# Performance work log

Measured on AMD Instinct MI355X. Metric: run time of the kernel, lower is better.

## Reference

```python
import jax, jax.numpy as jnp
import numpy as np

N = 100000
E = 3200000
F_IN, H1, H2, C = 512, 32, 16, 11


def setup_inputs() -> dict:
    key = jax.random.key(0)
    ks = jax.random.split(key, 8)
    x = jax.random.normal(ks[0], (N, F_IN), dtype=jnp.float32)
    edge_index = jax.random.randint(ks[1], (2, E), 0, N, dtype=jnp.int64)
    def glorot(k, fan_in, fan_out):
        lim = np.sqrt(6.0 / (fan_in + fan_out)).astype(np.float32)
        return jax.random.uniform(k, (fan_in, fan_out), jnp.float32, -lim, lim)
    return {
        "x": x,
        "edge_index": edge_index,
        "W1": glorot(ks[2], F_IN, H1), "b1": jnp.zeros((H1,), jnp.float32),
        "W2": glorot(ks[3], H1, H2),   "b2": jnp.zeros((H2,), jnp.float32),
        "W3": glorot(ks[4], H2, C),    "b3": jnp.zeros((C,), jnp.float32),
    }


def _gcn_conv(x, W, b, src, dst, deg_inv_sqrt):
    # GCNConv: D^{-1/2}(A+I)D^{-1/2} X W + b, self-loops handled analytically.
    h = x @ W                                   # [N, out]
    norm = deg_inv_sqrt[src] * deg_inv_sqrt[dst]  # [E]
    msg = h[src] * norm[:, None]                # gather + scale
    agg = jax.ops.segment_sum(msg, dst, num_segments=x.shape[0])
    agg = agg + h * (deg_inv_sqrt ** 2)[:, None]  # self-loop term
    return agg + b


def reference(x, edge_index, W1, b1, W2, b2, W3, b3):
    src, dst = edge_index[0], edge_index[1]
    n = x.shape[0]
    # degree with self-loops, counted on destination (PyG convention)
    deg = jax.ops.segment_sum(jnp.ones((dst.shape[0],), x.dtype), dst, num_segments=n) + 1.0
    deg_inv_sqrt = jax.lax.rsqrt(deg)
    h = jax.nn.relu(_gcn_conv(x, W1, b1, src, dst, deg_inv_sqrt))
    # F.dropout(training=self.training) is identity in eval mode
    h = jax.nn.relu(_gcn_conv(h, W2, b2, src, dst, deg_inv_sqrt))
    h = _gcn_conv(h, W3, b3, src, dst, deg_inv_sqrt)
    return jax.nn.log_softmax(h, axis=1)
```

## Files before the change

### kernel.cpp

```cpp
#include <hip/hip_runtime.h>
#include <hip/hip_bf16.h>

static __device__ __forceinline__ unsigned short f2bf(float f) {
    unsigned u = __float_as_uint(f);
    unsigned r = (u + 0x7FFF + ((u >> 16) & 1)) >> 16;
    return (unsigned short)r;
}
static __device__ __forceinline__ float bflo(unsigned v) { return __uint_as_float(v << 16); }
static __device__ __forceinline__ float bfhi(unsigned v) { return __uint_as_float(v & 0xFFFF0000u); }
static __device__ __forceinline__ unsigned pack2bf(float a, float b) {
    __hip_bfloat162 h2 = __float22bfloat162_rn(float2{a, b});
    union { __hip_bfloat162 h; unsigned u; } cv;
    cv.h = h2;
    return cv.u;
}

typedef __attribute__((ext_vector_type(8))) short bf16x8;
typedef __attribute__((ext_vector_type(8))) unsigned short u16x8;
typedef __attribute__((ext_vector_type(4))) float f32x4;

#define BKT_SHIFT 7
#define BKT_NODES 128
#define CHUNK 16384

__global__ __launch_bounds__(512) void hist_k(const int* __restrict__ dst, int* __restrict__ histG,
                                              int B, int NB, int E) {
    __shared__ int hist[1024];
    int tid = threadIdx.x;
    for (int i = tid; i < NB; i += 512) hist[i] = 0;
    __syncthreads();
    int base = blockIdx.x * CHUNK;
    for (int i = tid; i < CHUNK; i += 512) {
        int e = base + i;
        if (e >= E) break;
        atomicAdd(&hist[dst[e] >> BKT_SHIFT], 1);
    }
    __syncthreads();
    for (int i = tid; i < NB; i += 512) histG[(size_t)i * B + blockIdx.x] = hist[i];
}

__global__ __launch_bounds__(512) void scatter_k(const int* __restrict__ src, const int* __restrict__ dst,
                                                 const int* __restrict__ scanG, const int* __restrict__ blksum,
                                                 int* __restrict__ pairs, int B, int NB, int E) {
    __shared__ int sbase[1024];
    __shared__ int scnt[1024];
    int tid = threadIdx.x;
    for (int i = tid; i < NB; i += 512) {
        size_t idx = (size_t)i * B + blockIdx.x;
        sbase[i] = scanG[idx] + blksum[idx >> 11];
        scnt[i] = 0;
    }
    __syncthreads();
    int base = blockIdx.x * CHUNK;
    for (int i = tid; i < CHUNK; i += 512) {
        int e = base + i;
        if (e >= E) break;
        int d = dst[e], s = src[e];
        int b = d >> BKT_SHIFT;
        int r = atomicAdd(&scnt[b], 1);
        pairs[sbase[b] + r] = (s << BKT_SHIFT) | (d & (BKT_NODES - 1));
    }
}

#define SCAN_VPT 8
#define SCAN_ELEMS 2048

__global__ __launch_bounds__(256) void scan1(const int* __restrict__ in, int* __restrict__ out,
                                             int* __restrict__ blksum, int n) {
    __shared__ int sh[256];
    int base = blockIdx.x * SCAN_ELEMS + threadIdx.x * SCAN_VPT;
    int v[SCAN_VPT];
    int sum = 0;
    #pragma unroll
    for (int j = 0; j < SCAN_VPT; ++j) {
        v[j] = (base + j < n) ? in[base + j] : 0;
        sum += v[j];
    }
    sh[threadIdx.x] = sum;
    __syncthreads();
    for (int off = 1; off < 256; off <<= 1) {
        int t = (threadIdx.x >= off) ? sh[threadIdx.x - off] : 0;
        __syncthreads();
        sh[threadIdx.x] += t;
        __syncthreads();
    }
    if (threadIdx.x == 255) blksum[blockIdx.x] = sh[255];
    int run = sh[threadIdx.x] - sum;
    #pragma unroll
    for (int j = 0; j < SCAN_VPT; ++j) {
        if (base + j < n) out[base + j] = run;
        run += v[j];
    }
}

__global__ __launch_bounds__(256) void scan2(int* __restrict__ blksum, int nb) {
    __shared__ int sh[256];
    int t = threadIdx.x;
    int v = (t < nb) ? blksum[t] : 0;
    sh[t] = v;
    __syncthreads();
    for (int off = 1; off < 256; off <<= 1) {
        int u = (t >= off) ? sh[t - off] : 0;
        __syncthreads();
        sh[t] += u;
        __syncthreads();
    }
    if (t < nb) blksum[t] = sh[t] - v;
}

__global__ __launch_bounds__(256) void wconv(const float* __restrict__ W, unsigned short* __restrict__ W1T) {
    int gidx = blockIdx.x * 256 + threadIdx.x;
    if (gidx < 32 * 512) {
        int c = gidx >> 9, k = gidx & 511;
        W1T[gidx] = f2bf(W[(size_t)k * 32 + c]);
    }
}

#define SORT_CAP 8192

__global__ __launch_bounds__(512) void sort_bucket(const int* __restrict__ pairs,
        const int* __restrict__ scanG, const int* __restrict__ blksum, int B, int NB,
        int* __restrict__ csr_src, int* __restrict__ node_start,
        int* __restrict__ cnt, float* __restrict__ dis, int n, int E) {
    __shared__ int keys[SORT_CAP];
    __shared__ int lcnt[BKT_NODES];
    __shared__ int lscan[BKT_NODES];
    __shared__ int lfill[BKT_NODES];
    int bkt = blockIdx.x, tid = threadIdx.x;
    size_t idx0 = (size_t)bkt * B;
    int e0 = scanG[idx0] + blksum[idx0 >> 11];
    int e1 = E;
    if (bkt + 1 < NB) {
        size_t idx1 = (size_t)(bkt + 1) * B;
        e1 = scanG[idx1] + blksum[idx1 >> 11];
    }
    int m = e1 - e0;
    if (tid < BKT_NODES) { lcnt[tid] = 0; lfill[tid] = 0; }
    __syncthreads();
    for (int i = tid; i < m; i += 512) {
        int k = pairs[e0 + i];
        if (i < SORT_CAP) keys[i] = k;
        atomicAdd(&lcnt[k & (BKT_NODES - 1)], 1);
    }
    __syncthreads();
    if (tid < 64) {
        int c0 = lcnt[2 * tid], c1 = lcnt[2 * tid + 1];
        int s = c0 + c1;
        #pragma unroll
        for (int off = 1; off < 64; off <<= 1) {
            int t = __shfl_up(s, off);
            if (tid >= off) s += t;
        }
        lscan[2 * tid]     = s - c1 - c0;
        lscan[2 * tid + 1] = s - c1;
    }
    __syncthreads();
    int nb0 = bkt << BKT_SHIFT;
    if (tid < BKT_NODES && nb0 + tid < n) {
        int deg = lcnt[tid];
        node_start[nb0 + tid] = e0 + lscan[tid];
        cnt[nb0 + tid] = deg;
        dis[nb0 + tid] = rsqrtf((float)deg + 1.0f);
    }
    for (int i = tid; i < m; i += 512) {
        int k = (i < SORT_CAP) ? keys[i] : pairs[e0 + i];
        int d = k & (BKT_NODES - 1);
        int pos = lscan[d] + atomicAdd(&lfill[d], 1);
        csr_src[e0 + pos] = k >> BKT_SHIFT;
    }
}


__global__ __launch_bounds__(256) void gemm1_mfma(const float* __restrict__ x, const unsigned short* __restrict__ W1T,
                                                  const float* __restrict__ dis, unsigned short* __restrict__ g, int n) {
    __shared__ __attribute__((aligned(16))) unsigned short wT[32][520];
    int tid = threadIdx.x;
    int node0 = blockIdx.x * 64;

    #pragma unroll
    for (int r = 0; r < 8; ++r) {
        int u8 = tid + r * 256;
        int c = u8 >> 6, kq = (u8 & 63) * 8;
        *(u16x8*)(&wT[c][kq]) = *(const u16x8*)(W1T + (size_t)c * 512 + kq);
    }

    int wv_ = tid >> 6;
    int lane = tid & 63;
    int mrow = lane & 15;
    int kg = lane >> 4;
    int lnode = node0 + wv_ * 16 + mrow;
    int gn = min(lnode, n - 1);
    const float* xrow = x + (size_t)gn * 512 + kg * 8;
    f32x4 acc0 = {0.f, 0.f, 0.f, 0.f};
    f32x4 acc1 = {0.f, 0.f, 0.f, 0.f};
    __syncthreads();

    #pragma unroll 4
    for (int k0 = 0; k0 < 512; k0 += 32) {
        float4 xa = *(const float4*)(xrow + k0);
        float4 xc = *(const float4*)(xrow + k0 + 4);
        union { unsigned u[4]; bf16x8 v; } a;
        a.u[0] = pack2bf(xa.x, xa.y);
        a.u[1] = pack2bf(xa.z, xa.w);
        a.u[2] = pack2bf(xc.x, xc.y);
        a.u[3] = pack2bf(xc.z, xc.w);
        bf16x8 b0 = *(const bf16x8*)(&wT[mrow][k0 + kg * 8]);
        bf16x8 b1 = *(const bf16x8*)(&wT[16 + mrow][k0 + kg * 8]);
        acc0 = __builtin_amdgcn_mfma_f32_16x16x32_bf16(a.v, b0, acc0, 0, 0, 0);
        acc1 = __builtin_amdgcn_mfma_f32_16x16x32_bf16(a.v, b1, acc1, 0, 0, 0);
    }
    #pragma unroll
    for (int j = 0; j < 4; ++j) {
        int node = node0 + wv_ * 16 + kg * 4 + j;
        if (node < n) {
            float dv = dis[node];
            g[(size_t)node * 32 + mrow]      = f2bf(acc0[j] * dv);
            g[(size_t)node * 32 + 16 + mrow] = f2bf(acc1[j] * dv);
        }
    }
}


__global__ __launch_bounds__(256) void gather1(const int* __restrict__ csr_src,
        const int* __restrict__ start, const int* __restrict__ cnt,
        const unsigned short* __restrict__ g1, const float* __restrict__ dis,
        const float* __restrict__ b1, const float* __restrict__ W2,
        unsigned short* __restrict__ g2, int n) {
    __shared__ float w2t[16 * 33];
    for (int i = threadIdx.x; i < 512; i += 256) {
        int k = i >> 4, c = i & 15;
        w2t[c * 33 + k] = W2[i];
    }
    __syncthreads();
    int node = blockIdx.x * 4 + (threadIdx.x >> 6);
    if (node >= n) return;
    int lane = threadIdx.x & 63;
    int fq = lane & 7;
    int j = lane >> 3;
    int i0 = start[node], i1 = i0 + cnt[node];
    float a0 = 0.f, a1 = 0.f, a2 = 0.f, a3 = 0.f;
    int i = i0 + j;
    for (; i + 24 < i1; i += 32) {
        int s1 = csr_src[i];
        int s2 = csr_src[i + 8];
        int s3 = csr_src[i + 16];
        int s4 = csr_src[i + 24];
        uint2 v1 = *(const uint2*)(g1 + (size_t)s1 * 32 + fq * 4);
        uint2 v2 = *(const uint2*)(g1 + (size_t)s2 * 32 + fq * 4);
        uint2 v3 = *(const uint2*)(g1 + (size_t)s3 * 32 + fq * 4);
        uint2 v4 = *(const uint2*)(g1 + (size_t)s4 * 32 + fq * 4);
        a0 += bflo(v1.x) + bflo(v2.x) + bflo(v3.x) + bflo(v4.x);
        a1 += bfhi(v1.x) + bfhi(v2.x) + bfhi(v3.x) + bfhi(v4.x);
        a2 += bflo(v1.y) + bflo(v2.y) + bflo(v3.y) + bflo(v4.y);
        a3 += bfhi(v1.y) + bfhi(v2.y) + bfhi(v3.y) + bfhi(v4.y);
    }
    for (; i < i1; i += 8) {
        uint2 v = *(const uint2*)(g1 + (size_t)csr_src[i] * 32 + fq * 4);
        a0 += bflo(v.x); a1 += bfhi(v.x);
        a2 += bflo(v.y); a3 += bfhi(v.y);
    }
    #pragma unroll
    for (int m = 8; m < 64; m <<= 1) {
        a0 += __shfl_xor(a0, m); a1 += __shfl_xor(a1, m);
        a2 += __shfl_xor(a2, m); a3 += __shfl_xor(a3, m);
    }
    float dv = dis[node];
    uint2 sv = *(const uint2*)(g1 + (size_t)node * 32 + fq * 4);
    float v0 = fmaxf((a0 + bflo(sv.x)) * dv + b1[4 * fq + 0], 0.f);
    float v1f = fmaxf((a1 + bfhi(sv.x)) * dv + b1[4 * fq + 1], 0.f);
    float v2f = fmaxf((a2 + bflo(sv.y)) * dv + b1[4 * fq + 2], 0.f);
    float v3f = fmaxf((a3 + bfhi(sv.y)) * dv + b1[4 * fq + 3], 0.f);
    int c = lane & 15;
    int j3 = lane >> 4;
    float p = 0.f;
    #pragma unroll
    for (int kk = 0; kk < 8; ++kk) {
        int k = j3 * 8 + kk;
        int srcl = k >> 2;
        float xk;
        if ((kk & 3) == 0) xk = __shfl(v0, srcl);
        else if ((kk & 3) == 1) xk = __shfl(v1f, srcl);
        else if ((kk & 3) == 2) xk = __shfl(v2f, srcl);
        else xk = __shfl(v3f, srcl);
        p = fmaf(xk, w2t[c * 33 + k], p);
    }
    p += __shfl_xor(p, 16);
    p += __shfl_xor(p, 32);
    if (lane < 16) g2[(size_t)node * 16 + c] = f2bf(p * dv);
}


__global__ __launch_bounds__(256) void gather2(const int* __restrict__ csr_src,
        const int* __restrict__ start, const int* __restrict__ cnt,
        const unsigned short* __restrict__ g2, const float* __restrict__ dis,
        const float* __restrict__ b2, const float* __restrict__ W3,
        unsigned short* __restrict__ g3, int n) {
    __shared__ float w3t[16 * 17];
    if (threadIdx.x < 256) {
        int k = threadIdx.x >> 4, c = threadIdx.x & 15;
        w3t[c * 17 + k] = (c < 11) ? W3[(size_t)k * 11 + c] : 0.f;
    }
    __syncthreads();
    int node = blockIdx.x * 4 + (threadIdx.x >> 6);
    if (node >= n) return;
    int lane = threadIdx.x & 63;
    int fq = lane & 3;
    int j = lane >> 2;
    int i0 = start[node], i1 = i0 + cnt[node];
    float a0 = 0.f, a1 = 0.f, a2 = 0.f, a3 = 0.f;
    int i = i0 + j;
    for (; i + 16 < i1; i += 32) {
        int s1 = csr_src[i];
        int s2 = csr_src[i + 16];
        uint2 v1 = *(const uint2*)(g2 + (size_t)s1 * 16 + fq * 4);
        uint2 v2 = *(const uint2*)(g2 + (size_t)s2 * 16 + fq * 4);
        a0 += bflo(v1.x) + bflo(v2.x);
        a1 += bfhi(v1.x) + bfhi(v2.x);
        a2 += bflo(v1.y) + bflo(v2.y);
        a3 += bfhi(v1.y) + bfhi(v2.y);
    }
    if (i < i1) {
        uint2 v = *(const uint2*)(g2 + (size_t)csr_src[i] * 16 + fq * 4);
        a0 += bflo(v.x); a1 += bfhi(v.x);
        a2 += bflo(v.y); a3 += bfhi(v.y);
    }
    #pragma unroll
    for (int m = 4; m < 64; m <<= 1) {
        a0 += __shfl_xor(a0, m); a1 += __shfl_xor(a1, m);
        a2 += __shfl_xor(a2, m); a3 += __shfl_xor(a3, m);
    }
    float dv = dis[node];
    uint2 sv = *(const uint2*)(g2 + (size_t)node * 16 + fq * 4);
    float v0 = fmaxf((a0 + bflo(sv.x)) * dv + b2[4 * fq + 0], 0.f);
    float v1f = fmaxf((a1 + bfhi(sv.x)) * dv + b2[4 * fq + 1], 0.f);
    float v2f = fmaxf((a2 + bflo(sv.y)) * dv + b2[4 * fq + 2], 0.f);
    float v3f = fmaxf((a3 + bfhi(sv.y)) * dv + b2[4 * fq + 3], 0.f);
    int c = lane & 15;
    int j2 = lane >> 4;
    float p = 0.f;
    {
        float xk0 = __shfl(v0, j2);
        float xk1 = __shfl(v1f, j2);
        float xk2 = __shfl(v2f, j2);
        float xk3 = __shfl(v3f, j2);
        p = fmaf(xk0, w3t[c * 17 + j2 * 4 + 0], p);
        p = fmaf(xk1, w3t[c * 17 + j2 * 4 + 1], p);
        p = fmaf(xk2, w3t[c * 17 + j2 * 4 + 2], p);
        p = fmaf(xk3, w3t[c * 17 + j2 * 4 + 3], p);
    }
    p += __shfl_xor(p, 16);
    p += __shfl_xor(p, 32);
    if (lane < 16) g3[(size_t)node * 16 + c] = f2bf(p * dv);
}


__global__ __launch_bounds__(256) void gather3(const int* __restrict__ csr_src,
        const int* __restrict__ start, const int* __restrict__ cnt,
        const unsigned short* __restrict__ g, const float* __restrict__ dis,
        const float* __restrict__ bias, float* __restrict__ out, int n) {
    int node = blockIdx.x * 4 + (threadIdx.x >> 6);
    if (node >= n) return;
    int lane = threadIdx.x & 63;
    int fq = lane & 3;
    int j = lane >> 2;
    int i0 = start[node], i1 = i0 + cnt[node];
    float a0 = 0.f, a1 = 0.f, a2 = 0.f, a3 = 0.f;
    int i = i0 + j;
    for (; i + 16 < i1; i += 32) {
        int s1 = csr_src[i];
        int s2 = csr_src[i + 16];
        uint2 v1 = *(const uint2*)(g + (size_t)s1 * 16 + fq * 4);
        uint2 v2 = *(const uint2*)(g + (size_t)s2 * 16 + fq * 4);
        a0 += bflo(v1.x) + bflo(v2.x);
        a1 += bfhi(v1.x) + bfhi(v2.x);
        a2 += bflo(v1.y) + bflo(v2.y);
        a3 += bfhi(v1.y) + bfhi(v2.y);
    }
    if (i < i1) {
        uint2 v = *(const uint2*)(g + (size_t)csr_src[i] * 16 + fq * 4);
        a0 += bflo(v.x); a1 += bfhi(v.x);
        a2 += bflo(v.y); a3 += bfhi(v.y);
    }
    #pragma unroll
    for (int m = 4; m < 64; m <<= 1) {
        a0 += __shfl_xor(a0, m); a1 += __shfl_xor(a1, m);
        a2 += __shfl_xor(a2, m); a3 += __shfl_xor(a3, m);
    }
    float dvn = dis[node];
    uint2 sv = *(const uint2*)(g + (size_t)node * 16 + fq * 4);
    int f0 = 4 * fq;
    bool ok0 = f0 + 0 < 11, ok1 = f0 + 1 < 11, ok2 = f0 + 2 < 11, ok3 = f0 + 3 < 11;
    float v0 = (a0 + bflo(sv.x)) * dvn + (ok0 ? bias[f0 + 0] : 0.f);
    float v1f = (a1 + bfhi(sv.x)) * dvn + (ok1 ? bias[f0 + 1] : 0.f);
    float v2f = (a2 + bflo(sv.y)) * dvn + (ok2 ? bias[f0 + 2] : 0.f);
    float v3f = (a3 + bfhi(sv.y)) * dvn + (ok3 ? bias[f0 + 3] : 0.f);
    const float NEG = -3.0e38f;
    float m0 = fmaxf(fmaxf(ok0 ? v0 : NEG, ok1 ? v1f : NEG),
                     fmaxf(ok2 ? v2f : NEG, ok3 ? v3f : NEG));
    m0 = fmaxf(m0, __shfl_xor(m0, 1));
    m0 = fmaxf(m0, __shfl_xor(m0, 2));
    float s = (ok0 ? __expf(v0 - m0) : 0.f) + (ok1 ? __expf(v1f - m0) : 0.f)
            + (ok2 ? __expf(v2f - m0) : 0.f) + (ok3 ? __expf(v3f - m0) : 0.f);
    s += __shfl_xor(s, 1);
    s += __shfl_xor(s, 2);
    float ls = __logf(s) + m0;
    if (lane < 4) {
        float* orow = out + (size_t)node * 11 + f0;
        if (ok0) orow[0] = v0 - ls;
        if (ok1) orow[1] = v1f - ls;
        if (ok2) orow[2] = v2f - ls;
        if (ok3) orow[3] = v3f - ls;
    }
}


extern "C" void kernel_launch(void* const* d_in, const int* in_sizes, int n_in,
                              void* d_out, int out_size, void* d_ws, size_t ws_size,
                              hipStream_t stream) {
    const float* x  = (const float*)d_in[0];
    const int*   ei = (const int*)d_in[1];
    const float* W1 = (const float*)d_in[2];
    const float* b1 = (const float*)d_in[3];
    const float* W2 = (const float*)d_in[4];
    const float* b2 = (const float*)d_in[5];
    const float* W3 = (const float*)d_in[6];
    const float* b3 = (const float*)d_in[7];
    float* out = (float*)d_out;

    const int n = in_sizes[0] / 512;
    const int E = in_sizes[1] / 2;
    const int* src = ei;
    const int* dst = ei + E;

    const int NB = (n + BKT_NODES - 1) >> BKT_SHIFT;
    const int B  = (E + CHUNK - 1) / CHUNK;
    const int NBB = NB * B;
    const int nb_scan = (NBB + SCAN_ELEMS - 1) / SCAN_ELEMS;

    int* ws0 = (int*)d_ws;
    size_t off = 0;
    int*   cnt     = ws0 + off; off += (size_t)n;
    float* dis     = (float*)(ws0 + off); off += (size_t)n;
    int*   nstart  = ws0 + off; off += (size_t)n;
    int*   scanG   = ws0 + off; off += (size_t)NBB;
    int*   blksum  = ws0 + off; off += 256;
    int*   pairs   = ws0 + off; off += (size_t)E;
    int*   csr_src = ws0 + off; off += (size_t)E;
    unsigned short* g1 = (unsigned short*)(ws0 + off); off += (size_t)n * 16;
    unsigned short* g2 = (unsigned short*)(ws0 + off); off += (size_t)n * 8;
    unsigned short* g3 = (unsigned short*)(ws0 + off); off += (size_t)n * 8;
    unsigned short* W1T = (unsigned short*)(ws0 + off); off += 8192;
    int*   histG   = (int*)g1;

    hist_k<<<B, 512, 0, stream>>>(dst, histG, B, NB, E);
    scan1<<<nb_scan, 256, 0, stream>>>(histG, scanG, blksum, NBB);
    scan2<<<1, 256, 0, stream>>>(blksum, nb_scan);
    wconv<<<64, 256, 0, stream>>>(W1, W1T);
    scatter_k<<<B, 512, 0, stream>>>(src, dst, scanG, blksum, pairs, B, NB, E);
    sort_bucket<<<NB, 512, 0, stream>>>(pairs, scanG, blksum, B, NB, csr_src, nstart, cnt, dis, n, E);

    gemm1_mfma<<<(n + 63) / 64, 256, 0, stream>>>(x, W1T, dis, g1, n);
    gather1<<<(n + 3) / 4, 256, 0, stream>>>(csr_src, nstart, cnt, g1, dis, b1, W2, g2, n);
    gather2<<<(n + 3) / 4, 256, 0, stream>>>(csr_src, nstart, cnt, g2, dis, b2, W3, g3, n);
    gather3<<<(n + 3) / 4, 256, 0, stream>>>(csr_src, nstart, cnt, g3, dis, b3, out, n);
}
```

Measured before the change: 286.1 us.

## Co-schedule edge scatter with layer-1 GEMM and defer degree scaling to sort

Merges the edge-scatter pass and the layer-1 MFMA GEMM into one launch, split by block index, so the atomic-latency-bound scatter overlaps with the bandwidth-bound GEMM. To break the GEMM's dependence on degrees, the GEMM now writes unscaled bf16 rows. sort_bucket then rescales each bucket's g1 rows by D^-1/2 after computing degrees. The W1 bf16 transpose is folded into the histogram kernel as extra blocks, which cuts two launches. In exchange, g1 gets an extra read-modify-write and a second bf16 rounding, and the GEMM tile grows to 128 nodes per 512-thread block.

```diff
diff --git a/kernel.cpp b/kernel.cpp
--- a/kernel.cpp
+++ b/kernel.cpp
@@ -23,8 +23,17 @@
 #define BKT_NODES 128
 #define CHUNK 16384
 
-__global__ __launch_bounds__(512) void hist_k(const int* __restrict__ dst, int* __restrict__ histG,
-                                              int B, int NB, int E) {
+__global__ __launch_bounds__(512) void hist_wconv(const int* __restrict__ dst, int* __restrict__ histG,
+                                                  const float* __restrict__ W, unsigned short* __restrict__ W1T,
+                                                  int B, int NB, int E) {
+    if ((int)blockIdx.x >= B) {
+        int gidx = (blockIdx.x - B) * 512 + threadIdx.x;
+        if (gidx < 32 * 512) {
+            int c = gidx >> 9, k = gidx & 511;
+            W1T[gidx] = f2bf(W[(size_t)k * 32 + c]);
+        }
+        return;
+    }
     __shared__ int hist[1024];
     int tid = threadIdx.x;
     for (int i = tid; i < NB; i += 512) hist[i] = 0;
@@ -37,29 +46,6 @@
     }
     __syncthreads();
     for (int i = tid; i < NB; i += 512) histG[(size_t)i * B + blockIdx.x] = hist[i];
-}
-
-__global__ __launch_bounds__(512) void scatter_k(const int* __restrict__ src, const int* __restrict__ dst,
-                                                 const int* __restrict__ scanG, const int* __restrict__ blksum,
-                                                 int* __restrict__ pairs, int B, int NB, int E) {
-    __shared__ int sbase[1024];
-    __shared__ int scnt[1024];
-    int tid = threadIdx.x;
-    for (int i = tid; i < NB; i += 512) {
-        size_t idx = (size_t)i * B + blockIdx.x;
-        sbase[i] = scanG[idx] + blksum[idx >> 11];
-        scnt[i] = 0;
-    }
-    __syncthreads();
-    int base = blockIdx.x * CHUNK;
-    for (int i = tid; i < CHUNK; i += 512) {
-        int e = base + i;
-        if (e >= E) break;
-        int d = dst[e], s = src[e];
-        int b = d >> BKT_SHIFT;
-        int r = atomicAdd(&scnt[b], 1);
-        pairs[sbase[b] + r] = (s << BKT_SHIFT) | (d & (BKT_NODES - 1));
-    }
 }
 
 #define SCAN_VPT 8
@@ -108,78 +94,45 @@
     if (t < nb) blksum[t] = sh[t] - v;
 }
 
-__global__ __launch_bounds__(256) void wconv(const float* __restrict__ W, unsigned short* __restrict__ W1T) {
-    int gidx = blockIdx.x * 256 + threadIdx.x;
-    if (gidx < 32 * 512) {
-        int c = gidx >> 9, k = gidx & 511;
-        W1T[gidx] = f2bf(W[(size_t)k * 32 + c]);
-    }
-}
-
-#define SORT_CAP 8192
-
-__global__ __launch_bounds__(512) void sort_bucket(const int* __restrict__ pairs,
-        const int* __restrict__ scanG, const int* __restrict__ blksum, int B, int NB,
-        int* __restrict__ csr_src, int* __restrict__ node_start,
-        int* __restrict__ cnt, float* __restrict__ dis, int n, int E) {
-    __shared__ int keys[SORT_CAP];
-    __shared__ int lcnt[BKT_NODES];
-    __shared__ int lscan[BKT_NODES];
-    __shared__ int lfill[BKT_NODES];
-    int bkt = blockIdx.x, tid = threadIdx.x;
-    size_t idx0 = (size_t)bkt * B;
-    int e0 = scanG[idx0] + blksum[idx0 >> 11];
-    int e1 = E;
-    if (bkt + 1 < NB) {
-        size_t idx1 = (size_t)(bkt + 1) * B;
-        e1 = scanG[idx1] + blksum[idx1 >> 11];
-    }
-    int m = e1 - e0;
-    if (tid < BKT_NODES) { lcnt[tid] = 0; lfill[tid] = 0; }
-    __syncthreads();
-    for (int i = tid; i < m; i += 512) {
-        int k = pairs[e0 + i];
-        if (i < SORT_CAP) keys[i] = k;
-        atomicAdd(&lcnt[k & (BKT_NODES - 1)], 1);
-    }
-    __syncthreads();
-    if (tid < 64) {
-        int c0 = lcnt[2 * tid], c1 = lcnt[2 * tid + 1];
-        int s = c0 + c1;
-        #pragma unroll
-        for (int off = 1; off < 64; off <<= 1) {
-            int t = __shfl_up(s, off);
-            if (tid >= off) s += t;
-        }
-        lscan[2 * tid]     = s - c1 - c0;
-        lscan[2 * tid + 1] = s - c1;
-    }
-    __syncthreads();
-    int nb0 = bkt << BKT_SHIFT;
-    if (tid < BKT_NODES && nb0 + tid < n) {
-        int deg = lcnt[tid];
-        node_start[nb0 + tid] = e0 + lscan[tid];
-        cnt[nb0 + tid] = deg;
-        dis[nb0 + tid] = rsqrtf((float)deg + 1.0f);
-    }
-    for (int i = tid; i < m; i += 512) {
-        int k = (i < SORT_CAP) ? keys[i] : pairs[e0 + i];
-        int d = k & (BKT_NODES - 1);
-        int pos = lscan[d] + atomicAdd(&lfill[d], 1);
-        csr_src[e0 + pos] = k >> BKT_SHIFT;
-    }
-}
-
-
-__global__ __launch_bounds__(256) void gemm1_mfma(const float* __restrict__ x, const unsigned short* __restrict__ W1T,
-                                                  const float* __restrict__ dis, unsigned short* __restrict__ g, int n) {
-    __shared__ __attribute__((aligned(16))) unsigned short wT[32][520];
+
+__global__ __launch_bounds__(512) void scatter_gemm(const int* __restrict__ src, const int* __restrict__ dst,
+                                                    const int* __restrict__ scanG, const int* __restrict__ blksum,
+                                                    int* __restrict__ pairs,
+                                                    const float* __restrict__ x, const unsigned short* __restrict__ W1T,
+                                                    unsigned short* __restrict__ g1,
+                                                    int B, int NB, int E, int n) {
+    __shared__ __attribute__((aligned(16))) unsigned char lds_raw[32 * 520 * 2];
     int tid = threadIdx.x;
-    int node0 = blockIdx.x * 64;
-
-    #pragma unroll
-    for (int r = 0; r < 8; ++r) {
-        int u8 = tid + r * 256;
+
+    if ((int)blockIdx.x < B) {
+        int* sbase = (int*)lds_raw;
+        int* scnt  = (int*)(lds_raw + 4096);
+        for (int i = tid; i < NB; i += 512) {
+            size_t idx = (size_t)i * B + blockIdx.x;
+            sbase[i] = scanG[idx] + blksum[idx >> 11];
+            scnt[i] = 0;
+        }
+        __syncthreads();
+        int base = blockIdx.x * CHUNK;
+        for (int i = tid; i < CHUNK; i += 512) {
+            int e = base + i;
+            if (e >= E) break;
+            int d = dst[e], s = src[e];
+            int b = d >> BKT_SHIFT;
+            int r = atomicAdd(&scnt[b], 1);
+            pairs[sbase[b] + r] = (s << BKT_SHIFT) | (d & (BKT_NODES - 1));
+        }
+        return;
+    }
+
+    typedef unsigned short wrow_t[520];
+    wrow_t* wT = (wrow_t*)lds_raw;
+    int bid = blockIdx.x - B;
+    int node0 = bid * 128;
+
+    #pragma unroll
+    for (int r = 0; r < 4; ++r) {
+        int u8 = tid + r * 512;
         int c = u8 >> 6, kq = (u8 & 63) * 8;
         *(u16x8*)(&wT[c][kq]) = *(const u16x8*)(W1T + (size_t)c * 512 + kq);
     }
@@ -213,10 +166,81 @@
     for (int j = 0; j < 4; ++j) {
         int node = node0 + wv_ * 16 + kg * 4 + j;
         if (node < n) {
-            float dv = dis[node];
-            g[(size_t)node * 32 + mrow]      = f2bf(acc0[j] * dv);
-            g[(size_t)node * 32 + 16 + mrow] = f2bf(acc1[j] * dv);
-        }
+            g1[(size_t)node * 32 + mrow]      = f2bf(acc0[j]);
+            g1[(size_t)node * 32 + 16 + mrow] = f2bf(acc1[j]);
+        }
+    }
+}
+
+#define SORT_CAP 8192
+
+__global__ __launch_bounds__(512) void sort_bucket(const int* __restrict__ pairs,
+        const int* __restrict__ scanG, const int* __restrict__ blksum, int B, int NB,
+        int* __restrict__ csr_src, int* __restrict__ node_start,
+        int* __restrict__ cnt, float* __restrict__ dis,
+        unsigned short* __restrict__ g1, int n, int E) {
+    __shared__ int keys[SORT_CAP];
+    __shared__ int lcnt[BKT_NODES];
+    __shared__ int lscan[BKT_NODES];
+    __shared__ int lfill[BKT_NODES];
+    __shared__ float sdis[BKT_NODES];
+    int bkt = blockIdx.x, tid = threadIdx.x;
+    size_t idx0 = (size_t)bkt * B;
+    int e0 = scanG[idx0] + blksum[idx0 >> 11];
+    int e1 = E;
+    if (bkt + 1 < NB) {
+        size_t idx1 = (size_t)(bkt + 1) * B;
+        e1 = scanG[idx1] + blksum[idx1 >> 11];
+    }
+    int m = e1 - e0;
+    if (tid < BKT_NODES) { lcnt[tid] = 0; lfill[tid] = 0; }
+    __syncthreads();
+    for (int i = tid; i < m; i += 512) {
+        int k = pairs[e0 + i];
+        if (i < SORT_CAP) keys[i] = k;
+        atomicAdd(&lcnt[k & (BKT_NODES - 1)], 1);
+    }
+    __syncthreads();
+    if (tid < 64) {
+        int c0 = lcnt[2 * tid], c1 = lcnt[2 * tid + 1];
+        int s = c0 + c1;
+        #pragma unroll
+        for (int off = 1; off < 64; off <<= 1) {
+            int t = __shfl_up(s, off);
+            if (tid >= off) s += t;
+        }
+        lscan[2 * tid]     = s - c1 - c0;
+        lscan[2 * tid + 1] = s - c1;
+    }
+    __syncthreads();
+    int nb0 = bkt << BKT_SHIFT;
+    if (tid < BKT_NODES) {
+        int deg = lcnt[tid];
+        float d = rsqrtf((float)deg + 1.0f);
+        sdis[tid] = d;
+        if (nb0 + tid < n) {
+            node_start[nb0 + tid] = e0 + lscan[tid];
+            cnt[nb0 + tid] = deg;
+            dis[nb0 + tid] = d;
+        }
+    }
+    for (int i = tid; i < m; i += 512) {
+        int k = (i < SORT_CAP) ? keys[i] : pairs[e0 + i];
+        int d = k & (BKT_NODES - 1);
+        int pos = lscan[d] + atomicAdd(&lfill[d], 1);
+        csr_src[e0 + pos] = k >> BKT_SHIFT;
+    }
+    __syncthreads();
+    for (int i = tid; i < 1024; i += 512) {
+        int row = i >> 3;
+        int node = nb0 + row;
+        if (node >= n) break;
+        float dvv = sdis[row];
+        unsigned short* rp = g1 + (size_t)node * 32 + (i & 7) * 4;
+        uint2 v = *(uint2*)rp;
+        v.x = pack2bf(bflo(v.x) * dvv, bfhi(v.x) * dvv);
+        v.y = pack2bf(bflo(v.y) * dvv, bfhi(v.y) * dvv);
+        *(uint2*)rp = v;
     }
 }
 
@@ -452,14 +476,13 @@
     unsigned short* W1T = (unsigned short*)(ws0 + off); off += 8192;
     int*   histG   = (int*)g1;
 
-    hist_k<<<B, 512, 0, stream>>>(dst, histG, B, NB, E);
+    hist_wconv<<<B + 32, 512, 0, stream>>>(dst, histG, W1, W1T, B, NB, E);
     scan1<<<nb_scan, 256, 0, stream>>>(histG, scanG, blksum, NBB);
     scan2<<<1, 256, 0, stream>>>(blksum, nb_scan);
-    wconv<<<64, 256, 0, stream>>>(W1, W1T);
-    scatter_k<<<B, 512, 0, stream>>>(src, dst, scanG, blksum, pairs, B, NB, E);
-    sort_bucket<<<NB, 512, 0, stream>>>(pairs, scanG, blksum, B, NB, csr_src, nstart, cnt, dis, n, E);
-
-    gemm1_mfma<<<(n + 63) / 64, 256, 0, stream>>>(x, W1T, dis, g1, n);
+    scatter_gemm<<<B + (n + 127) / 128, 512, 0, stream>>>(src, dst, scanG, blksum, pairs,
+                                                          x, W1T, g1, B, NB, E, n);
+    sort_bucket<<<NB, 512, 0, stream>>>(pairs, scanG, blksum, B, NB, csr_src, nstart, cnt, dis, g1, n, E);
+
     gather1<<<(n + 3) / 4, 256, 0, stream>>>(csr_src, nstart, cnt, g1, dis, b1, W2, g2, n);
     gather2<<<(n + 3) / 4, 256, 0, stream>>>(csr_src, nstart, cnt, g2, dis, b2, W3, g3, n);
     gather3<<<(n + 3) / 4, 256, 0, stream>>>(csr_src, nstart, cnt, g3, dis, b3, out, n);
```

After: 282.1 us. Within noise of the previous version (-1.4%).

## Stage x tiles through LDS in gemm1 and fuse weight conversion into histogram

Applied to the files above, without the earlier changes.

The first-layer GEMM now has 512-thread blocks covering 128 nodes. Each block loads x in coalesced 64-column slabs, converts them to bf16 into shared memory, and feeds the MFMAs from LDS. Before, each lane issued strided per-row float4 loads, so this targets global-load coalescing on the 200MB x read. The separate W1 transpose/convert kernel is folded into the histogram launch as extra blocks, removing one launch. The trade-off is two barriers per k-step and more LDS per block, which may lower occupancy and overlap.

```diff
diff --git a/kernel.cpp b/kernel.cpp
--- a/kernel.cpp
+++ b/kernel.cpp
@@ -23,8 +23,17 @@
 #define BKT_NODES 128
 #define CHUNK 16384
 
-__global__ __launch_bounds__(512) void hist_k(const int* __restrict__ dst, int* __restrict__ histG,
-                                              int B, int NB, int E) {
+__global__ __launch_bounds__(512) void hist_wconv(const int* __restrict__ dst, int* __restrict__ histG,
+                                                  const float* __restrict__ W, unsigned short* __restrict__ W1T,
+                                                  int B, int NB, int E) {
+    if ((int)blockIdx.x >= B) {
+        int gidx = (blockIdx.x - B) * 512 + threadIdx.x;
+        if (gidx < 32 * 512) {
+            int c = gidx >> 9, k = gidx & 511;
+            W1T[gidx] = f2bf(W[(size_t)k * 32 + c]);
+        }
+        return;
+    }
     __shared__ int hist[1024];
     int tid = threadIdx.x;
     for (int i = tid; i < NB; i += 512) hist[i] = 0;
@@ -106,14 +115,6 @@
         __syncthreads();
     }
     if (t < nb) blksum[t] = sh[t] - v;
-}
-
-__global__ __launch_bounds__(256) void wconv(const float* __restrict__ W, unsigned short* __restrict__ W1T) {
-    int gidx = blockIdx.x * 256 + threadIdx.x;
-    if (gidx < 32 * 512) {
-        int c = gidx >> 9, k = gidx & 511;
-        W1T[gidx] = f2bf(W[(size_t)k * 32 + c]);
-    }
 }
 
 #define SORT_CAP 8192
@@ -171,15 +172,16 @@
 }
 
 
-__global__ __launch_bounds__(256) void gemm1_mfma(const float* __restrict__ x, const unsigned short* __restrict__ W1T,
+__global__ __launch_bounds__(512) void gemm1_mfma(const float* __restrict__ x, const unsigned short* __restrict__ W1T,
                                                   const float* __restrict__ dis, unsigned short* __restrict__ g, int n) {
     __shared__ __attribute__((aligned(16))) unsigned short wT[32][520];
+    __shared__ __attribute__((aligned(16))) unsigned short xb[128][72];
     int tid = threadIdx.x;
-    int node0 = blockIdx.x * 64;
-
-    #pragma unroll
-    for (int r = 0; r < 8; ++r) {
-        int u8 = tid + r * 256;
+    int node0 = blockIdx.x * 128;
+
+    #pragma unroll
+    for (int r = 0; r < 4; ++r) {
+        int u8 = tid + r * 512;
         int c = u8 >> 6, kq = (u8 & 63) * 8;
         *(u16x8*)(&wT[c][kq]) = *(const u16x8*)(W1T + (size_t)c * 512 + kq);
     }
@@ -188,26 +190,31 @@
     int lane = tid & 63;
     int mrow = lane & 15;
     int kg = lane >> 4;
-    int lnode = node0 + wv_ * 16 + mrow;
-    int gn = min(lnode, n - 1);
-    const float* xrow = x + (size_t)gn * 512 + kg * 8;
     f32x4 acc0 = {0.f, 0.f, 0.f, 0.f};
     f32x4 acc1 = {0.f, 0.f, 0.f, 0.f};
-    __syncthreads();
-
-    #pragma unroll 4
-    for (int k0 = 0; k0 < 512; k0 += 32) {
-        float4 xa = *(const float4*)(xrow + k0);
-        float4 xc = *(const float4*)(xrow + k0 + 4);
-        union { unsigned u[4]; bf16x8 v; } a;
-        a.u[0] = pack2bf(xa.x, xa.y);
-        a.u[1] = pack2bf(xa.z, xa.w);
-        a.u[2] = pack2bf(xc.x, xc.y);
-        a.u[3] = pack2bf(xc.z, xc.w);
-        bf16x8 b0 = *(const bf16x8*)(&wT[mrow][k0 + kg * 8]);
-        bf16x8 b1 = *(const bf16x8*)(&wT[16 + mrow][k0 + kg * 8]);
-        acc0 = __builtin_amdgcn_mfma_f32_16x16x32_bf16(a.v, b0, acc0, 0, 0, 0);
-        acc1 = __builtin_amdgcn_mfma_f32_16x16x32_bf16(a.v, b1, acc1, 0, 0, 0);
+
+    for (int k0 = 0; k0 < 512; k0 += 64) {
+        __syncthreads();
+        #pragma unroll
+        for (int r = 0; r < 4; ++r) {
+            int fi = tid + r * 512;
+            int nd = fi >> 4, kq = (fi & 15) * 4;
+            int gn = min(node0 + nd, n - 1);
+            float4 xv = *(const float4*)(x + (size_t)gn * 512 + k0 + kq);
+            uint2 pw;
+            pw.x = pack2bf(xv.x, xv.y);
+            pw.y = pack2bf(xv.z, xv.w);
+            *(uint2*)(&xb[nd][kq]) = pw;
+        }
+        __syncthreads();
+        #pragma unroll
+        for (int ks = 0; ks < 2; ++ks) {
+            bf16x8 a  = *(const bf16x8*)(&xb[wv_ * 16 + mrow][ks * 32 + kg * 8]);
+            bf16x8 b0 = *(const bf16x8*)(&wT[mrow][k0 + ks * 32 + kg * 8]);
+            bf16x8 b1 = *(const bf16x8*)(&wT[16 + mrow][k0 + ks * 32 + kg * 8]);
+            acc0 = __builtin_amdgcn_mfma_f32_16x16x32_bf16(a, b0, acc0, 0, 0, 0);
+            acc1 = __builtin_amdgcn_mfma_f32_16x16x32_bf16(a, b1, acc1, 0, 0, 0);
+        }
     }
     #pragma unroll
     for (int j = 0; j < 4; ++j) {
@@ -452,14 +459,13 @@
     unsigned short* W1T = (unsigned short*)(ws0 + off); off += 8192;
     int*   histG   = (int*)g1;
 
-    hist_k<<<B, 512, 0, stream>>>(dst, histG, B, NB, E);
+    hist_wconv<<<B + 32, 512, 0, stream>>>(dst, histG, W1, W1T, B, NB, E);
     scan1<<<nb_scan, 256, 0, stream>>>(histG, scanG, blksum, NBB);
     scan2<<<1, 256, 0, stream>>>(blksum, nb_scan);
-    wconv<<<64, 256, 0, stream>>>(W1, W1T);
     scatter_k<<<B, 512, 0, stream>>>(src, dst, scanG, blksum, pairs, B, NB, E);
     sort_bucket<<<NB, 512, 0, stream>>>(pairs, scanG, blksum, B, NB, csr_src, nstart, cnt, dis, n, E);
 
-    gemm1_mfma<<<(n + 63) / 64, 256, 0, stream>>>(x, W1T, dis, g1, n);
+    gemm1_mfma<<<(n + 127) / 128, 512, 0, stream>>>(x, W1T, dis, g1, n);
     gather1<<<(n + 3) / 4, 256, 0, stream>>>(csr_src, nstart, cnt, g1, dis, b1, W2, g2, n);
     gather2<<<(n + 3) / 4, 256, 0, stream>>>(csr_src, nstart, cnt, g2, dis, b2, W3, g3, n);
     gather3<<<(n + 3) / 4, 256, 0, stream>>>(csr_src, nstart, cnt, g3, dis, b3, out, n);
```

New measurement: 283.1 us. No clear change (-1.1%).
